# Optimization experiments

Measured on AMD Instinct MI355X. Metric: run time of the kernel, lower is better.

Reference implementation:

```python
import jax, jax.numpy as jnp
import numpy as np

NUM_HEADS = 32

def setup_inputs() -> dict:
    key = jax.random.key(0)
    k1, k2, k3 = jax.random.split(key, 3)
    B, C, H, W = 4, 768, 32, 32
    x = jax.random.normal(k1, (B, C, H, W), dtype=jnp.float32)
    # 1x1 conv kernels represented as [C_in, C_out] matrices
    w_qkv = jax.random.normal(k2, (C, 3 * C), dtype=jnp.float32) * (2.0 / (3 * C)) ** 0.5
    b_qkv = jnp.zeros((3 * C,), dtype=jnp.float32)
    w_proj = jax.random.normal(k3, (C, C), dtype=jnp.float32) * (2.0 / C) ** 0.5
    b_proj = jnp.zeros((C,), dtype=jnp.float32)
    return {"x": x, "w_qkv": w_qkv, "b_qkv": b_qkv, "w_proj": w_proj, "b_proj": b_proj}

def reference(x, w_qkv, b_qkv, w_proj, b_proj):
    B, C, H, W = x.shape
    h = NUM_HEADS
    hd = C // h
    scale = hd ** (-0.5)
    # qkv 1x1 conv (channels_first): [B,C,H,W] -> [B,3C,H,W]
    qkv = jnp.einsum('bchw,cd->bdhw', x, w_qkv) + b_qkv[None, :, None, None]
    qkv = qkv.reshape(B, 3, h, hd, H * W)
    q = qkv[:, 0]  # [B,h,hd,HW]
    k = qkv[:, 1]  # [B,h,hd,HW]
    v = qkv[:, 2]  # [B,h,hd,HW]
    # attn = q^T @ k : [B,h,HW,HW]
    attn = jnp.einsum('bhdq,bhdk->bhqk', q, k) * scale
    attn = jax.nn.softmax(attn, axis=-1)
    # out = (attn @ v^T)^T : [B,h,hd,HW]
    o = jnp.einsum('bhqk,bhdk->bhdq', attn, v)
    o = o.reshape(B, C, H, W)
    # proj 1x1 conv
    out = jnp.einsum('bchw,cf->bfhw', o, w_proj) + b_proj[None, :, None, None]
    return out
```

## Files before the change

### kernel.cpp

```cpp
#include <hip/hip_runtime.h>
#include <hip/hip_bf16.h>

#define B_  4
#define C_  768
#define N_  1024
#define NH  32
#define HD  24
#define HDP 32
#define D3  2304
#define QSCALE 0.29448889f

typedef __hip_bfloat16 bf16;
typedef __attribute__((ext_vector_type(8))) short bf16x8;
typedef __attribute__((ext_vector_type(4))) float f32x4;

__device__ __forceinline__ unsigned cvt_pk_bf16(float lo, float hi) {
    unsigned r;
    asm volatile("v_cvt_pk_bf16_f32 %0, %1, %2" : "=v"(r) : "v"(lo), "v"(hi));
    return r;
}

__device__ __forceinline__ float fast_exp2(float x) {
    float r;
    asm volatile("v_exp_f32 %0, %1" : "=v"(r) : "v"(x));
    return r;
}

__device__ __forceinline__ void gload_lds16(const bf16* g, bf16* l) {
    __builtin_amdgcn_global_load_lds(
        (const __attribute__((address_space(1))) void*)g,
        (__attribute__((address_space(3))) void*)l, 16, 0, 0);
}

__global__ __launch_bounds__(256) void transpose_cvt(
        const float* __restrict__ in, bf16* __restrict__ out,
        int R, int Cc, long inb, long outb) {
    __shared__ float tile[32][33];
    const int b = blockIdx.z;
    const float* src = in + (size_t)b * inb;
    bf16* dst = out + (size_t)b * outb;
    const int r0 = blockIdx.y * 32, c0 = blockIdx.x * 32;
    const int tx = threadIdx.x, ty = threadIdx.y;
    #pragma unroll
    for (int k = 0; k < 4; k++)
        tile[ty + 8*k][tx] = src[(size_t)(r0 + ty + 8*k) * Cc + c0 + tx];
    __syncthreads();
    #pragma unroll
    for (int k = 0; k < 4; k++)
        dst[(size_t)(c0 + ty + 8*k) * R + r0 + tx] = __float2bfloat16(tile[tx][ty + 8*k]);
}

__global__ __launch_bounds__(256) void fill_ones(bf16* __restrict__ vB) {
    bf16* row = vB + ((size_t)blockIdx.x * HDP + 24) * N_;
    const ushort4 ones = {0x3F80, 0x3F80, 0x3F80, 0x3F80};
    *(ushort4*)&row[threadIdx.x * 4] = ones;
}

template<int MODE>
__global__ __launch_bounds__(256) void gemm_mfma(
        const bf16* __restrict__ xt, const bf16* __restrict__ wqT,
        const bf16* __restrict__ wpT, const bf16* __restrict__ obuf,
        const float* __restrict__ bqkv, const float* __restrict__ bproj,
        bf16* __restrict__ qT, bf16* __restrict__ kT, bf16* __restrict__ vB,
        float* __restrict__ outF) {
    __shared__ bf16 As[128 * 32];
    __shared__ bf16 Bs[128 * 32];

    const int b = blockIdx.z;
    const bf16* Ap; const bf16* Bp;
    if (MODE == 0) { Ap = xt + (size_t)b * N_ * C_;   Bp = wqT; }
    if (MODE == 1) { Ap = wqT + (size_t)1536 * C_;    Bp = xt + (size_t)b * N_ * C_; }
    if (MODE == 2) { Ap = wpT;                        Bp = obuf + (size_t)b * N_ * C_; }

    const int t = threadIdx.x;
    const int lane = t & 63, wid = t >> 6;
    const int c = lane & 15, g = lane >> 4;
    const int wm = wid >> 1, wn = wid & 1;
    const int M0 = blockIdx.x * 128, Nc0 = blockIdx.y * 128;

    const int srow = lane >> 2, schunk = lane & 3;
    const bf16* Ag0 = Ap + (size_t)(M0 + wid * 32 + srow) * C_ + schunk * 8;
    const bf16* Ag1 = Ag0 + 16 * C_;
    const bf16* Bg0 = Bp + (size_t)(Nc0 + wid * 32 + srow) * C_ + schunk * 8;
    const bf16* Bg1 = Bg0 + 16 * C_;
    bf16* lA0 = &As[(wid * 32) * 32];
    bf16* lA1 = &As[(wid * 32 + 16) * 32];
    bf16* lB0 = &Bs[(wid * 32) * 32];
    bf16* lB1 = &Bs[(wid * 32 + 16) * 32];

    f32x4 acc[4][4];
    #pragma unroll
    for (int i = 0; i < 4; i++)
        #pragma unroll
        for (int j = 0; j < 4; j++) acc[i][j] = f32x4{0.f, 0.f, 0.f, 0.f};

    for (int k0 = 0; k0 < C_; k0 += 32) {
        __syncthreads();
        gload_lds16(Ag0 + k0, lA0);
        gload_lds16(Ag1 + k0, lA1);
        gload_lds16(Bg0 + k0, lB0);
        gload_lds16(Bg1 + k0, lB1);
        __syncthreads();

        bf16x8 af[4], bfr[4];
        #pragma unroll
        for (int mi = 0; mi < 4; mi++)
            af[mi] = *(const bf16x8*)&As[(wm * 64 + mi * 16 + c) * 32 + g * 8];
        #pragma unroll
        for (int ni = 0; ni < 4; ni++)
            bfr[ni] = *(const bf16x8*)&Bs[(wn * 64 + ni * 16 + c) * 32 + g * 8];
        #pragma unroll
        for (int mi = 0; mi < 4; mi++)
            #pragma unroll
            for (int ni = 0; ni < 4; ni++)
                acc[mi][ni] = __builtin_amdgcn_mfma_f32_16x16x32_bf16(
                    af[mi], bfr[ni], acc[mi][ni], 0, 0, 0);
    }

    const int row0 = M0 + wm * 64, col0 = Nc0 + wn * 64;
    if (MODE == 0) {
        #pragma unroll
        for (int ni = 0; ni < 4; ni++) {
            const int j = col0 + ni * 16 + c;
            const int issec = j >= 768;
            bf16* dstbase = issec ? kT : qT;
            const int dd = j - (issec ? 768 : 0);
            const int hh = dd / 24, hd = dd % 24;
            const float bq = bqkv[j];
            const float sca = issec ? 1.0f : QSCALE;
            #pragma unroll
            for (int mi = 0; mi < 4; mi++)
                #pragma unroll
                for (int r = 0; r < 4; r++) {
                    const int n = row0 + mi * 16 + 4 * g + r;
                    dstbase[(((size_t)(b * NH + hh) * N_) + n) * HDP + hd] =
                        __float2bfloat16((acc[mi][ni][r] + bq) * sca);
                }
        }
    } else if (MODE == 1) {
        #pragma unroll
        for (int mi = 0; mi < 4; mi++)
            #pragma unroll
            for (int r = 0; r < 4; r++) {
                const int vd = row0 + mi * 16 + 4 * g + r;
                const int hh = vd / 24, hd = vd % 24;
                const float bq = bqkv[1536 + vd];
                #pragma unroll
                for (int ni = 0; ni < 4; ni++) {
                    const int n = col0 + ni * 16 + c;
                    vB[((size_t)(b * NH + hh) * HDP + hd) * N_ + n] =
                        __float2bfloat16(acc[mi][ni][r] + bq);
                }
            }
    } else {
        #pragma unroll
        for (int mi = 0; mi < 4; mi++)
            #pragma unroll
            for (int r = 0; r < 4; r++) {
                const int f = row0 + mi * 16 + 4 * g + r;
                const float bp = bproj[f];
                #pragma unroll
                for (int ni = 0; ni < 4; ni++) {
                    const int n = col0 + ni * 16 + c;
                    outF[((size_t)b * C_ + f) * N_ + n] = acc[mi][ni][r] + bp;
                }
            }
    }
}

__global__ __launch_bounds__(256) void attn_mfma(
        const bf16* __restrict__ qT, const bf16* __restrict__ kT,
        const bf16* __restrict__ vB, bf16* __restrict__ obuf) {
    __shared__ bf16 Ps[4][32 * 72];
    const int t = threadIdx.x, lane = t & 63, wid = t >> 6;
    const int c = lane & 15, g = lane >> 4;
    const int bid = blockIdx.x;
    const int xcd = bid & 7, idx = bid >> 3;
    const int hl = xcd * 16 + (idx & 15);
    const int qb = idx >> 4;
    const int b = hl >> 5, h = hl & 31;
    const int q0 = qb * 128 + wid * 32;
    const size_t hb = (size_t)(b * NH + h);
    const bf16* qh = qT + hb * N_ * HDP;
    const bf16* kh = kT + hb * N_ * HDP;
    const bf16* vh = vB + hb * HDP * N_;
    bf16* myPs = &Ps[wid][0];

    const bf16x8 qf0 = *(const bf16x8*)(qh + (size_t)(q0 + c) * HDP + g * 8);
    const bf16x8 qf1 = *(const bf16x8*)(qh + (size_t)(q0 + 16 + c) * HDP + g * 8);
    f32x4 o00 = {0.f,0.f,0.f,0.f}, o01 = {0.f,0.f,0.f,0.f};
    f32x4 o10 = {0.f,0.f,0.f,0.f}, o11 = {0.f,0.f,0.f,0.f};
    const bf16* vrowA = vh + (size_t)c * N_;
    const bf16* vrowB = vh + (size_t)(16 + c) * N_;

    for (int k0 = 0; k0 < N_; k0 += 64) {
        f32x4 st0[4], st1[4];
        #pragma unroll
        for (int tt = 0; tt < 4; tt++) {
            bf16x8 kf = *(const bf16x8*)(kh + (size_t)(k0 + tt * 16 + c) * HDP + g * 8);
            f32x4 z = {0.f, 0.f, 0.f, 0.f};
            st0[tt] = __builtin_amdgcn_mfma_f32_16x16x32_bf16(kf, qf0, z, 0, 0, 0);
            st1[tt] = __builtin_amdgcn_mfma_f32_16x16x32_bf16(kf, qf1, z, 0, 0, 0);
        }
        float p0[16], p1[16];
        #pragma unroll
        for (int tt = 0; tt < 4; tt++)
            #pragma unroll
            for (int r = 0; r < 4; r++) {
                p0[tt * 4 + r] = fast_exp2(st0[tt][r]);
                p1[tt * 4 + r] = fast_exp2(st1[tt][r]);
            }
        #pragma unroll
        for (int tt = 0; tt < 4; tt++) {
            uint2 w0, w1;
            w0.x = cvt_pk_bf16(p0[tt * 4 + 0], p0[tt * 4 + 1]);
            w0.y = cvt_pk_bf16(p0[tt * 4 + 2], p0[tt * 4 + 3]);
            w1.x = cvt_pk_bf16(p1[tt * 4 + 0], p1[tt * 4 + 1]);
            w1.y = cvt_pk_bf16(p1[tt * 4 + 2], p1[tt * 4 + 3]);
            *(uint2*)&myPs[c * 72 + tt * 16 + g * 4]        = w0;
            *(uint2*)&myPs[(16 + c) * 72 + tt * 16 + g * 4] = w1;
        }
        bf16x8 pa00 = *(const bf16x8*)&myPs[c * 72 + g * 8];
        bf16x8 pa01 = *(const bf16x8*)&myPs[c * 72 + 32 + g * 8];
        bf16x8 pa10 = *(const bf16x8*)&myPs[(16 + c) * 72 + g * 8];
        bf16x8 pa11 = *(const bf16x8*)&myPs[(16 + c) * 72 + 32 + g * 8];

        bf16x8 va0 = *(const bf16x8*)(vrowA + k0 + g * 8);
        bf16x8 va1 = *(const bf16x8*)(vrowA + k0 + 32 + g * 8);
        bf16x8 vb0 = *(const bf16x8*)(vrowB + k0 + g * 8);
        bf16x8 vb1 = *(const bf16x8*)(vrowB + k0 + 32 + g * 8);
        o00 = __builtin_amdgcn_mfma_f32_16x16x32_bf16(pa00, va0, o00, 0, 0, 0);
        o00 = __builtin_amdgcn_mfma_f32_16x16x32_bf16(pa01, va1, o00, 0, 0, 0);
        o01 = __builtin_amdgcn_mfma_f32_16x16x32_bf16(pa00, vb0, o01, 0, 0, 0);
        o01 = __builtin_amdgcn_mfma_f32_16x16x32_bf16(pa01, vb1, o01, 0, 0, 0);
        o10 = __builtin_amdgcn_mfma_f32_16x16x32_bf16(pa10, va0, o10, 0, 0, 0);
        o10 = __builtin_amdgcn_mfma_f32_16x16x32_bf16(pa11, va1, o10, 0, 0, 0);
        o11 = __builtin_amdgcn_mfma_f32_16x16x32_bf16(pa10, vb0, o11, 0, 0, 0);
        o11 = __builtin_amdgcn_mfma_f32_16x16x32_bf16(pa11, vb1, o11, 0, 0, 0);
    }

    float inv0[4], inv1[4];
    #pragma unroll
    for (int r = 0; r < 4; r++) {
        inv0[r] = 1.f / __shfl(o01[r], g * 16 + 8);
        inv1[r] = 1.f / __shfl(o11[r], g * 16 + 8);
    }
    #pragma unroll
    for (int dt = 0; dt < 2; dt++) {
        const int dcol = dt * 16 + c;
        if (dcol < HD) {
            const f32x4 oa = dt ? o01 : o00;
            const f32x4 ob = dt ? o11 : o10;
            #pragma unroll
            for (int r = 0; r < 4; r++) {
                const int qa = q0 + g * 4 + r;
                const int qb2 = q0 + 16 + g * 4 + r;
                obuf[((size_t)b * N_ + qa) * C_ + h * HD + dcol] =
                    __float2bfloat16(oa[r] * inv0[r]);
                obuf[((size_t)b * N_ + qb2) * C_ + h * HD + dcol] =
                    __float2bfloat16(ob[r] * inv1[r]);
            }
        }
    }
}

extern "C" void kernel_launch(void* const* d_in, const int* in_sizes, int n_in,
                              void* d_out, int out_size, void* d_ws, size_t ws_size,
                              hipStream_t stream) {
    const float* x      = (const float*)d_in[0];
    const float* w_qkv  = (const float*)d_in[1];
    const float* b_qkv  = (const float*)d_in[2];
    const float* w_proj = (const float*)d_in[3];
    const float* b_proj = (const float*)d_in[4];
    float* out = (float*)d_out;

    char* ws = (char*)d_ws;
    bf16* xt   = (bf16*)(ws);
    bf16* wqT  = (bf16*)(ws + 6291456);
    bf16* wpT  = (bf16*)(ws + 9830400);
    bf16* qT   = (bf16*)(ws + 11010048);
    bf16* kT   = (bf16*)(ws + 19398656);
    bf16* vB   = (bf16*)(ws + 27787264);
    bf16* obuf = (bf16*)(ws + 36175872);

    hipMemsetAsync(qT, 0, 8388608, stream);

    transpose_cvt<<<dim3(32, 24, 4), dim3(32, 8), 0, stream>>>(
        x, xt, 768, 1024, (long)768 * 1024, (long)1024 * 768);
    transpose_cvt<<<dim3(72, 24, 1), dim3(32, 8), 0, stream>>>(
        w_qkv, wqT, 768, 2304, 0, 0);
    transpose_cvt<<<dim3(24, 24, 1), dim3(32, 8), 0, stream>>>(
        w_proj, wpT, 768, 768, 0, 0);
    fill_ones<<<dim3(B_ * NH), 256, 0, stream>>>(vB);

    gemm_mfma<0><<<dim3(8, 12, 4), 256, 0, stream>>>(
        xt, wqT, wpT, obuf, b_qkv, b_proj, qT, kT, vB, nullptr);
    gemm_mfma<1><<<dim3(6, 8, 4), 256, 0, stream>>>(
        xt, wqT, wpT, obuf, b_qkv, b_proj, qT, kT, vB, nullptr);
    attn_mfma<<<dim3(1024), 256, 0, stream>>>(qT, kT, vB, obuf);
    gemm_mfma<2><<<dim3(6, 8, 4), 256, 0, stream>>>(
        xt, wqT, wpT, obuf, b_qkv, b_proj, qT, kT, vB, out);
}
```

Baseline: 191.4 us.

## Double-buffer GEMM and attention loads, merge QKV launches, retile projection GEMM

The QK and V projection GEMMs become one launch, with vmode chosen by blockIdx.y. Both GEMMs now double-buffer their LDS tiles, so the global-to-LDS load for the next K step overlaps the current MFMA work and each iteration needs one barrier instead of two. The projection GEMM uses 64x128 tiles, giving twice as many blocks and better occupancy across the CUs. The attention kernel now stages K and V tiles cooperatively in double-buffered LDS with register prefetch, replacing the per-wave scattered global loads. This costs more LDS per block, which may lower occupancy.

```diff
diff --git a/kernel.cpp b/kernel.cpp
--- a/kernel.cpp
+++ b/kernel.cpp
@@ -56,37 +56,34 @@
     *(ushort4*)&row[threadIdx.x * 4] = ones;
 }
 
-template<int MODE>
-__global__ __launch_bounds__(256) void gemm_mfma(
+__global__ __launch_bounds__(256) void gemm_qkv(
         const bf16* __restrict__ xt, const bf16* __restrict__ wqT,
-        const bf16* __restrict__ wpT, const bf16* __restrict__ obuf,
-        const float* __restrict__ bqkv, const float* __restrict__ bproj,
-        bf16* __restrict__ qT, bf16* __restrict__ kT, bf16* __restrict__ vB,
-        float* __restrict__ outF) {
-    __shared__ bf16 As[128 * 32];
-    __shared__ bf16 Bs[128 * 32];
+        const float* __restrict__ bqkv,
+        bf16* __restrict__ qT, bf16* __restrict__ kT, bf16* __restrict__ vB) {
+    __shared__ bf16 As[2][128 * 32];
+    __shared__ bf16 Bs[2][128 * 32];
 
     const int b = blockIdx.z;
-    const bf16* Ap; const bf16* Bp;
-    if (MODE == 0) { Ap = xt + (size_t)b * N_ * C_;   Bp = wqT; }
-    if (MODE == 1) { Ap = wqT + (size_t)1536 * C_;    Bp = xt + (size_t)b * N_ * C_; }
-    if (MODE == 2) { Ap = wpT;                        Bp = obuf + (size_t)b * N_ * C_; }
+    const bool vmode = (blockIdx.y >= 12);
+    const bf16* Ap; const bf16* Bp; int M0, Nc0;
+    if (!vmode) {
+        Ap = xt + (size_t)b * N_ * C_;  Bp = wqT;
+        M0 = blockIdx.x * 128;          Nc0 = blockIdx.y * 128;
+    } else {
+        Ap = wqT + (size_t)1536 * C_;   Bp = xt + (size_t)b * N_ * C_;
+        M0 = (blockIdx.y - 12) * 128;   Nc0 = blockIdx.x * 128;
+    }
 
     const int t = threadIdx.x;
     const int lane = t & 63, wid = t >> 6;
     const int c = lane & 15, g = lane >> 4;
     const int wm = wid >> 1, wn = wid & 1;
-    const int M0 = blockIdx.x * 128, Nc0 = blockIdx.y * 128;
 
     const int srow = lane >> 2, schunk = lane & 3;
     const bf16* Ag0 = Ap + (size_t)(M0 + wid * 32 + srow) * C_ + schunk * 8;
     const bf16* Ag1 = Ag0 + 16 * C_;
     const bf16* Bg0 = Bp + (size_t)(Nc0 + wid * 32 + srow) * C_ + schunk * 8;
     const bf16* Bg1 = Bg0 + 16 * C_;
-    bf16* lA0 = &As[(wid * 32) * 32];
-    bf16* lA1 = &As[(wid * 32 + 16) * 32];
-    bf16* lB0 = &Bs[(wid * 32) * 32];
-    bf16* lB1 = &Bs[(wid * 32 + 16) * 32];
 
     f32x4 acc[4][4];
     #pragma unroll
@@ -94,31 +91,40 @@
         #pragma unroll
         for (int j = 0; j < 4; j++) acc[i][j] = f32x4{0.f, 0.f, 0.f, 0.f};
 
-    for (int k0 = 0; k0 < C_; k0 += 32) {
-        __syncthreads();
-        gload_lds16(Ag0 + k0, lA0);
-        gload_lds16(Ag1 + k0, lA1);
-        gload_lds16(Bg0 + k0, lB0);
-        gload_lds16(Bg1 + k0, lB1);
-        __syncthreads();
-
+    gload_lds16(Ag0, &As[0][(wid * 32) * 32]);
+    gload_lds16(Ag1, &As[0][(wid * 32 + 16) * 32]);
+    gload_lds16(Bg0, &Bs[0][(wid * 32) * 32]);
+    gload_lds16(Bg1, &Bs[0][(wid * 32 + 16) * 32]);
+    __syncthreads();
+
+    int cur = 0;
+    for (int s = 0; s < 24; s++) {
+        if (s < 23) {
+            const int k1 = (s + 1) * 32;
+            gload_lds16(Ag0 + k1, &As[cur ^ 1][(wid * 32) * 32]);
+            gload_lds16(Ag1 + k1, &As[cur ^ 1][(wid * 32 + 16) * 32]);
+            gload_lds16(Bg0 + k1, &Bs[cur ^ 1][(wid * 32) * 32]);
+            gload_lds16(Bg1 + k1, &Bs[cur ^ 1][(wid * 32 + 16) * 32]);
+        }
         bf16x8 af[4], bfr[4];
         #pragma unroll
         for (int mi = 0; mi < 4; mi++)
-            af[mi] = *(const bf16x8*)&As[(wm * 64 + mi * 16 + c) * 32 + g * 8];
+            af[mi] = *(const bf16x8*)&As[cur][(wm * 64 + mi * 16 + c) * 32 + g * 8];
         #pragma unroll
         for (int ni = 0; ni < 4; ni++)
-            bfr[ni] = *(const bf16x8*)&Bs[(wn * 64 + ni * 16 + c) * 32 + g * 8];
+            bfr[ni] = *(const bf16x8*)&Bs[cur][(wn * 64 + ni * 16 + c) * 32 + g * 8];
         #pragma unroll
         for (int mi = 0; mi < 4; mi++)
             #pragma unroll
             for (int ni = 0; ni < 4; ni++)
                 acc[mi][ni] = __builtin_amdgcn_mfma_f32_16x16x32_bf16(
                     af[mi], bfr[ni], acc[mi][ni], 0, 0, 0);
+        __syncthreads();
+        cur ^= 1;
     }
 
     const int row0 = M0 + wm * 64, col0 = Nc0 + wn * 64;
-    if (MODE == 0) {
+    if (!vmode) {
         #pragma unroll
         for (int ni = 0; ni < 4; ni++) {
             const int j = col0 + ni * 16 + c;
@@ -137,7 +143,7 @@
                         __float2bfloat16((acc[mi][ni][r] + bq) * sca);
                 }
         }
-    } else if (MODE == 1) {
+    } else {
         #pragma unroll
         for (int mi = 0; mi < 4; mi++)
             #pragma unroll
@@ -152,26 +158,88 @@
                         __float2bfloat16(acc[mi][ni][r] + bq);
                 }
             }
-    } else {
-        #pragma unroll
-        for (int mi = 0; mi < 4; mi++)
-            #pragma unroll
-            for (int r = 0; r < 4; r++) {
-                const int f = row0 + mi * 16 + 4 * g + r;
-                const float bp = bproj[f];
-                #pragma unroll
-                for (int ni = 0; ni < 4; ni++) {
-                    const int n = col0 + ni * 16 + c;
-                    outF[((size_t)b * C_ + f) * N_ + n] = acc[mi][ni][r] + bp;
-                }
+    }
+}
+
+__global__ __launch_bounds__(256) void gemm_proj(
+        const bf16* __restrict__ wpT, const bf16* __restrict__ obuf,
+        const float* __restrict__ bproj, float* __restrict__ outF) {
+    __shared__ bf16 As[2][64 * 32];
+    __shared__ bf16 Bs[2][128 * 32];
+
+    const int b = blockIdx.z;
+    const bf16* Ap = wpT;
+    const bf16* Bp = obuf + (size_t)b * N_ * C_;
+    const int M0 = blockIdx.x * 64, Nc0 = blockIdx.y * 128;
+
+    const int t = threadIdx.x;
+    const int lane = t & 63, wid = t >> 6;
+    const int c = lane & 15, g = lane >> 4;
+    const int wm = wid >> 1, wn = wid & 1;
+
+    const int srow = lane >> 2, schunk = lane & 3;
+    const bf16* AgP = Ap + (size_t)(M0 + wid * 16 + srow) * C_ + schunk * 8;
+    const bf16* Bg0 = Bp + (size_t)(Nc0 + wid * 32 + srow) * C_ + schunk * 8;
+    const bf16* Bg1 = Bg0 + 16 * C_;
+
+    f32x4 acc[2][4];
+    #pragma unroll
+    for (int i = 0; i < 2; i++)
+        #pragma unroll
+        for (int j = 0; j < 4; j++) acc[i][j] = f32x4{0.f, 0.f, 0.f, 0.f};
+
+    gload_lds16(AgP, &As[0][(wid * 16) * 32]);
+    gload_lds16(Bg0, &Bs[0][(wid * 32) * 32]);
+    gload_lds16(Bg1, &Bs[0][(wid * 32 + 16) * 32]);
+    __syncthreads();
+
+    int cur = 0;
+    for (int s = 0; s < 24; s++) {
+        if (s < 23) {
+            const int k1 = (s + 1) * 32;
+            gload_lds16(AgP + k1, &As[cur ^ 1][(wid * 16) * 32]);
+            gload_lds16(Bg0 + k1, &Bs[cur ^ 1][(wid * 32) * 32]);
+            gload_lds16(Bg1 + k1, &Bs[cur ^ 1][(wid * 32 + 16) * 32]);
+        }
+        bf16x8 af[2], bfr[4];
+        #pragma unroll
+        for (int mi = 0; mi < 2; mi++)
+            af[mi] = *(const bf16x8*)&As[cur][(wm * 32 + mi * 16 + c) * 32 + g * 8];
+        #pragma unroll
+        for (int ni = 0; ni < 4; ni++)
+            bfr[ni] = *(const bf16x8*)&Bs[cur][(wn * 64 + ni * 16 + c) * 32 + g * 8];
+        #pragma unroll
+        for (int mi = 0; mi < 2; mi++)
+            #pragma unroll
+            for (int ni = 0; ni < 4; ni++)
+                acc[mi][ni] = __builtin_amdgcn_mfma_f32_16x16x32_bf16(
+                    af[mi], bfr[ni], acc[mi][ni], 0, 0, 0);
+        __syncthreads();
+        cur ^= 1;
+    }
+
+    const int row0 = M0 + wm * 32, col0 = Nc0 + wn * 64;
+    #pragma unroll
+    for (int mi = 0; mi < 2; mi++)
+        #pragma unroll
+        for (int r = 0; r < 4; r++) {
+            const int f = row0 + mi * 16 + 4 * g + r;
+            const float bp = bproj[f];
+            #pragma unroll
+            for (int ni = 0; ni < 4; ni++) {
+                const int n = col0 + ni * 16 + c;
+                outF[((size_t)b * C_ + f) * N_ + n] = acc[mi][ni][r] + bp;
             }
-    }
+        }
 }
 
 __global__ __launch_bounds__(256) void attn_mfma(
         const bf16* __restrict__ qT, const bf16* __restrict__ kT,
         const bf16* __restrict__ vB, bf16* __restrict__ obuf) {
+    __shared__ bf16 Kb[2][64 * 40];
+    __shared__ bf16 Vb[2][32 * 72];
     __shared__ bf16 Ps[4][32 * 72];
+
     const int t = threadIdx.x, lane = t & 63, wid = t >> 6;
     const int c = lane & 15, g = lane >> 4;
     const int bid = blockIdx.x;
@@ -190,14 +258,29 @@
     const bf16x8 qf1 = *(const bf16x8*)(qh + (size_t)(q0 + 16 + c) * HDP + g * 8);
     f32x4 o00 = {0.f,0.f,0.f,0.f}, o01 = {0.f,0.f,0.f,0.f};
     f32x4 o10 = {0.f,0.f,0.f,0.f}, o11 = {0.f,0.f,0.f,0.f};
-    const bf16* vrowA = vh + (size_t)c * N_;
-    const bf16* vrowB = vh + (size_t)(16 + c) * N_;
-
-    for (int k0 = 0; k0 < N_; k0 += 64) {
+
+    const bf16* kgp = kh + (size_t)(t >> 2) * HDP + (t & 3) * 8;
+    const bf16* vgp = vh + (size_t)(t >> 3) * N_ + (t & 7) * 8;
+    const int kws = (t >> 2) * 40 + (t & 3) * 8;
+    const int vws = (t >> 3) * 72 + (t & 7) * 8;
+
+    int4 rk = *(const int4*)kgp;
+    int4 rv = *(const int4*)vgp;
+    *(int4*)&Kb[0][kws] = rk;
+    *(int4*)&Vb[0][vws] = rv;
+    __syncthreads();
+
+    int cur = 0;
+    for (int kt = 0; kt < 16; kt++) {
+        if (kt < 15) {
+            const int k1 = (kt + 1) * 64;
+            rk = *(const int4*)(kgp + (size_t)k1 * HDP);
+            rv = *(const int4*)(vgp + k1);
+        }
         f32x4 st0[4], st1[4];
         #pragma unroll
         for (int tt = 0; tt < 4; tt++) {
-            bf16x8 kf = *(const bf16x8*)(kh + (size_t)(k0 + tt * 16 + c) * HDP + g * 8);
+            bf16x8 kf = *(const bf16x8*)&Kb[cur][(tt * 16 + c) * 40 + g * 8];
             f32x4 z = {0.f, 0.f, 0.f, 0.f};
             st0[tt] = __builtin_amdgcn_mfma_f32_16x16x32_bf16(kf, qf0, z, 0, 0, 0);
             st1[tt] = __builtin_amdgcn_mfma_f32_16x16x32_bf16(kf, qf1, z, 0, 0, 0);
@@ -225,10 +308,10 @@
         bf16x8 pa10 = *(const bf16x8*)&myPs[(16 + c) * 72 + g * 8];
         bf16x8 pa11 = *(const bf16x8*)&myPs[(16 + c) * 72 + 32 + g * 8];
 
-        bf16x8 va0 = *(const bf16x8*)(vrowA + k0 + g * 8);
-        bf16x8 va1 = *(const bf16x8*)(vrowA + k0 + 32 + g * 8);
-        bf16x8 vb0 = *(const bf16x8*)(vrowB + k0 + g * 8);
-        bf16x8 vb1 = *(const bf16x8*)(vrowB + k0 + 32 + g * 8);
+        bf16x8 va0 = *(const bf16x8*)&Vb[cur][c * 72 + g * 8];
+        bf16x8 va1 = *(const bf16x8*)&Vb[cur][c * 72 + 32 + g * 8];
+        bf16x8 vb0 = *(const bf16x8*)&Vb[cur][(16 + c) * 72 + g * 8];
+        bf16x8 vb1 = *(const bf16x8*)&Vb[cur][(16 + c) * 72 + 32 + g * 8];
         o00 = __builtin_amdgcn_mfma_f32_16x16x32_bf16(pa00, va0, o00, 0, 0, 0);
         o00 = __builtin_amdgcn_mfma_f32_16x16x32_bf16(pa01, va1, o00, 0, 0, 0);
         o01 = __builtin_amdgcn_mfma_f32_16x16x32_bf16(pa00, vb0, o01, 0, 0, 0);
@@ -237,6 +320,13 @@
         o10 = __builtin_amdgcn_mfma_f32_16x16x32_bf16(pa11, va1, o10, 0, 0, 0);
         o11 = __builtin_amdgcn_mfma_f32_16x16x32_bf16(pa10, vb0, o11, 0, 0, 0);
         o11 = __builtin_amdgcn_mfma_f32_16x16x32_bf16(pa11, vb1, o11, 0, 0, 0);
+
+        if (kt < 15) {
+            *(int4*)&Kb[cur ^ 1][kws] = rk;
+            *(int4*)&Vb[cur ^ 1][vws] = rv;
+        }
+        __syncthreads();
+        cur ^= 1;
     }
 
     float inv0[4], inv1[4];
@@ -293,11 +383,9 @@
         w_proj, wpT, 768, 768, 0, 0);
     fill_ones<<<dim3(B_ * NH), 256, 0, stream>>>(vB);
 
-    gemm_mfma<0><<<dim3(8, 12, 4), 256, 0, stream>>>(
-        xt, wqT, wpT, obuf, b_qkv, b_proj, qT, kT, vB, nullptr);
-    gemm_mfma<1><<<dim3(6, 8, 4), 256, 0, stream>>>(
-        xt, wqT, wpT, obuf, b_qkv, b_proj, qT, kT, vB, nullptr);
+    gemm_qkv<<<dim3(8, 18, 4), 256, 0, stream>>>(
+        xt, wqT, b_qkv, qT, kT, vB);
     attn_mfma<<<dim3(1024), 256, 0, stream>>>(qT, kT, vB, obuf);
-    gemm_mfma<2><<<dim3(6, 8, 4), 256, 0, stream>>>(
-        xt, wqT, wpT, obuf, b_qkv, b_proj, qT, kT, vB, out);
-}
+    gemm_proj<<<dim3(12, 8, 4), 256, 0, stream>>>(
+        wpT, obuf, b_proj, out);
+}
```

Measured after the change: 176.7 us. -7.7%, faster.
